# Optimization experiments

Hardware: AMD Instinct MI355X
Metric: run time of the kernel (lower is better)

## Reference

```python
import jax, jax.numpy as jnp
import numpy as np

B = 131072      # batch of states
N_ACT = 40      # output_dim (Tetris action space)


def setup_inputs() -> dict:
    key = jax.random.key(0)
    ks = jax.random.split(key, 9)
    # state vector: 11 real-valued board features, 1 hold-piece id in [0,4),
    # 3 next-piece ids in [1,8) (0 is treated as invalid by the original code)
    keep = jax.random.normal(ks[0], (B, 11), dtype=jnp.float32)
    hold = jax.random.randint(ks[1], (B, 1), 0, 4).astype(jnp.float32)
    nxt = jax.random.randint(ks[2], (B, 3), 1, 8).astype(jnp.float32)
    x = jnp.concatenate([keep, hold, nxt], axis=1)  # [B, 15]
    W1 = jax.random.normal(ks[3], (36, 128), dtype=jnp.float32) * 0.1
    b1 = jnp.zeros((128,), dtype=jnp.float32)
    W2 = jax.random.normal(ks[4], (128, 512), dtype=jnp.float32) * 0.05
    b2 = jnp.zeros((512,), dtype=jnp.float32)
    W4 = jax.random.normal(ks[5], (512, N_ACT), dtype=jnp.float32) * 0.05
    b4 = jnp.zeros((N_ACT,), dtype=jnp.float32)
    return {"x": x, "W1": W1, "b1": b1, "W2": W2, "b2": b2, "W4": W4, "b4": b4}


def reference(x, W1, b1, W2, b2, W4, b4):
    B_, _ = x.shape
    keep = x[:, :11]                                      # [B, 11]
    # vectorized replacement of the per-sample .item() one-hot loop
    hold_idx = jax.lax.stop_gradient(jnp.clip(x[:, 11].astype(jnp.int32), 0, 3))
    nxt_idx = jax.lax.stop_gradient(jnp.clip(x[:, 12:15].astype(jnp.int32) - 1, 0, 6))
    hold_oh = jax.nn.one_hot(hold_idx, 4, dtype=x.dtype)  # [B, 4]
    nxt_oh = jax.nn.one_hot(nxt_idx, 7, dtype=x.dtype).reshape(B_, 21)  # [B, 21]
    inp = jnp.concatenate([keep, hold_oh, nxt_oh], axis=1)  # [B, 36]
    h = jax.nn.relu(inp @ W1 + b1)   # [B, 128]
    h = jax.nn.relu(h @ W2 + b2)     # [B, 512]
    return h @ W4 + b4               # [B, N_ACT]
```

## Files before the change

kernel.cpp:

```cpp
#include <hip/hip_runtime.h>


typedef short bf16x8 __attribute__((ext_vector_type(8)));
typedef float f32x4 __attribute__((ext_vector_type(4)));
typedef unsigned int u32;

#define NW1F 8192
#define NW2F 65536
#define NW4F 24576
#define PACK_TOTAL (NW1F + NW2F + NW4F)
#define PACK_THREADS (PACK_TOTAL / 8)

__device__ __forceinline__ unsigned short f2bf(float f) {
  union { float f; unsigned u; } a; a.f = f;
  unsigned r = a.u + 0x7fffu + ((a.u >> 16) & 1u);
  return (unsigned short)(r >> 16);
}
__device__ __forceinline__ u32 cvtpk(float lo, float hi) {
  u32 r;
  asm("v_cvt_pk_bf16_f32 %0, %1, %2" : "=v"(r) : "v"(lo), "v"(hi));
  return r;
}

__global__ void pack_weights(const float* __restrict__ W1,
                             const float* __restrict__ W2,
                             const float* __restrict__ W4,
                             unsigned short* __restrict__ wf) {
  int t = blockIdx.x * 256 + threadIdx.x;
  if (t >= PACK_THREADS) return;
  int fid = t >> 6, lane = t & 63;
  int l16 = lane & 15, quad = lane >> 4;
  float vals[8];
  if (fid < 16) {
    int mt = fid >> 1, ks = fid & 1;
    int m = mt * 16 + l16, k0 = ks * 32 + quad * 8;
#pragma unroll
    for (int j = 0; j < 8; ++j) { int k = k0 + j; vals[j] = (k < 36) ? W1[k * 128 + m] : 0.f; }
  } else if (fid < 144) {
    int f = fid - 16, mt = f >> 2, ks = f & 3;
    int m = mt * 16 + l16, k0 = ks * 32 + quad * 8;
#pragma unroll
    for (int j = 0; j < 8; ++j) vals[j] = W2[(k0 + j) * 512 + m];
  } else {
    int f = fid - 144, mt = f >> 4, ks = f & 15;
    int m = mt * 16 + l16, k0 = ks * 32 + quad * 8;
#pragma unroll
    for (int j = 0; j < 8; ++j) vals[j] = (m < 40) ? W4[(k0 + j) * 40 + m] : 0.f;
  }
  u32 p[4];
#pragma unroll
  for (int j = 0; j < 4; ++j) p[j] = cvtpk(vals[2 * j], vals[2 * j + 1]);
  *(bf16x8*)(wf + (size_t)t * 8) = *(bf16x8*)p;
}

__global__ __launch_bounds__(128, 2) void dqn_fused(
    const float* __restrict__ x,
    const unsigned short* __restrict__ wf,
    const float* __restrict__ b1,
    const float* __restrict__ b2,
    const float* __restrict__ b4,
    float* __restrict__ out) {
  __shared__ __align__(16) unsigned short sBuf[2 * 64 * 72];

  const int tid  = threadIdx.x;
  const int lane = tid & 63;
  const int wave = tid >> 6;
  const int quad = lane >> 4;
  const int l16  = lane & 15;
  const int row0 = blockIdx.x << 7;
  const int lr0  = wave * 64;
  unsigned short* su = sBuf + wave * (64 * 72);

  const unsigned short* w2f = wf + NW1F;
  const unsigned short* w4f = wf + NW1F + NW2F;
  const unsigned short* w2p = w2f + lane * 8;

  bf16x8 curW[4];
#pragma unroll
  for (int k = 0; k < 4; ++k) curW[k] = *(const bf16x8*)(w2p + (size_t)k * 512);

  {
    const float* xr = x + (size_t)(row0 + lr0 + lane) * 15;
    unsigned short* dst = su + lane * 72;
    bf16x8 z = {0, 0, 0, 0, 0, 0, 0, 0};
#pragma unroll
    for (int c = 8; c < 64; c += 8) *(bf16x8*)(dst + c) = z;
    u32 p[4];
#pragma unroll
    for (int i = 0; i < 4; ++i) p[i] = cvtpk(xr[2 * i], xr[2 * i + 1]);
    *(bf16x8*)dst = *(bf16x8*)p;
    *(u32*)(dst + 8) = cvtpk(xr[8], xr[9]);
    dst[10] = f2bf(xr[10]);
    int hold = (int)xr[11]; hold = hold < 0 ? 0 : (hold > 3 ? 3 : hold);
    dst[11 + hold] = 0x3F80;
#pragma unroll
    for (int t = 0; t < 3; ++t) {
      int nx = (int)xr[12 + t] - 1; nx = nx < 0 ? 0 : (nx > 6 ? 6 : nx);
      dst[15 + t * 7 + nx] = 0x3F80;
    }
  }

  const f32x4 vzero = {0.f, 0.f, 0.f, 0.f};

  bf16x8 ib[4][2];
#pragma unroll
  for (int rg = 0; rg < 4; ++rg)
#pragma unroll
    for (int ks = 0; ks < 2; ++ks)
      ib[rg][ks] = *(const bf16x8*)(su + (rg * 16 + l16) * 72 + ks * 32 + quad * 8);

  bf16x8 af1[4][4];
#pragma unroll
  for (int half = 0; half < 2; ++half) {
    bf16x8 wa[4][2];
#pragma unroll
    for (int mtl = 0; mtl < 4; ++mtl)
#pragma unroll
      for (int ks = 0; ks < 2; ++ks)
        wa[mtl][ks] = *(const bf16x8*)(
            wf + (size_t)(((half * 4 + mtl) * 2 + ks) * 64 + lane) * 8);

    f32x4 acc1[4][4];
#pragma unroll
    for (int mtl = 0; mtl < 4; ++mtl)
#pragma unroll
      for (int rg = 0; rg < 4; ++rg) acc1[mtl][rg] = vzero;

#pragma unroll
    for (int mtl = 0; mtl < 4; ++mtl)
#pragma unroll
      for (int ks = 0; ks < 2; ++ks)
#pragma unroll
        for (int rg = 0; rg < 4; ++rg)
          acc1[mtl][rg] = __builtin_amdgcn_mfma_f32_16x16x32_bf16(wa[mtl][ks], ib[rg][ks], acc1[mtl][rg], 0, 0, 0);

#pragma unroll
    for (int mtl = 0; mtl < 4; ++mtl) {
      f32x4 bias = *(const f32x4*)(b1 + (half * 4 + mtl) * 16 + quad * 4);
#pragma unroll
      for (int rg = 0; rg < 4; ++rg) {
        float v0 = fmaxf(acc1[mtl][rg][0] + bias[0], 0.f);
        float v1 = fmaxf(acc1[mtl][rg][1] + bias[1], 0.f);
        float v2 = fmaxf(acc1[mtl][rg][2] + bias[2], 0.f);
        float v3 = fmaxf(acc1[mtl][rg][3] + bias[3], 0.f);
        uint2 pk = {cvtpk(v0, v1), cvtpk(v2, v3)};
        *(uint2*)(su + (rg * 16 + l16) * 72 + mtl * 16 + quad * 4) = pk;
      }
    }
#pragma unroll
    for (int rg = 0; rg < 4; ++rg)
#pragma unroll
      for (int ksl = 0; ksl < 2; ++ksl)
        af1[rg][half * 2 + ksl] =
            *(const bf16x8*)(su + (rg * 16 + l16) * 72 + ksl * 32 + quad * 8);
  }

  f32x4 accO[3][4];
#pragma unroll
  for (int mt = 0; mt < 3; ++mt)
#pragma unroll
    for (int rg = 0; rg < 4; ++rg) accO[mt][rg] = vzero;

  for (int chunk = 0; chunk < 8; ++chunk) {
    bf16x8 w4r[2][3];
#pragma unroll
    for (int ks3 = 0; ks3 < 2; ++ks3)
#pragma unroll
      for (int mt3 = 0; mt3 < 3; ++mt3)
        w4r[ks3][mt3] = *(const bf16x8*)(
            w4f + (size_t)((mt3 * 16 + chunk * 2 + ks3) * 64 + lane) * 8);

#pragma unroll
    for (int mtl = 0; mtl < 4; ++mtl) {
      int fb = chunk * 16 + mtl * 4 + 4;
      if (fb >= 128) fb = 0;
      bf16x8 nxtW[4];
#pragma unroll
      for (int k = 0; k < 4; ++k)
        nxtW[k] = *(const bf16x8*)(w2p + (size_t)(fb + k) * 512);

      f32x4 acc2[4];
#pragma unroll
      for (int rg = 0; rg < 4; ++rg) acc2[rg] = vzero;
#pragma unroll
      for (int ks = 0; ks < 4; ++ks)
#pragma unroll
        for (int rg = 0; rg < 4; ++rg)
          acc2[rg] = __builtin_amdgcn_mfma_f32_16x16x32_bf16(curW[ks], af1[rg][ks], acc2[rg], 0, 0, 0);

      f32x4 bias = *(const f32x4*)(b2 + chunk * 64 + mtl * 16 + quad * 4);
#pragma unroll
      for (int rg = 0; rg < 4; ++rg) {
        float v0 = fmaxf(acc2[rg][0] + bias[0], 0.f);
        float v1 = fmaxf(acc2[rg][1] + bias[1], 0.f);
        float v2 = fmaxf(acc2[rg][2] + bias[2], 0.f);
        float v3 = fmaxf(acc2[rg][3] + bias[3], 0.f);
        uint2 pk = {cvtpk(v0, v1), cvtpk(v2, v3)};
        *(uint2*)(su + (rg * 16 + l16) * 72 + mtl * 16 + quad * 4) = pk;
      }
#pragma unroll
      for (int k = 0; k < 4; ++k) curW[k] = nxtW[k];
    }

#pragma unroll
    for (int ks3 = 0; ks3 < 2; ++ks3) {
      bf16x8 h[4];
#pragma unroll
      for (int rg = 0; rg < 4; ++rg)
        h[rg] = *(const bf16x8*)(su + (rg * 16 + l16) * 72 + ks3 * 32 + quad * 8);
#pragma unroll
      for (int mt3 = 0; mt3 < 3; ++mt3)
#pragma unroll
        for (int rg = 0; rg < 4; ++rg)
          accO[mt3][rg] = __builtin_amdgcn_mfma_f32_16x16x32_bf16(w4r[ks3][mt3], h[rg], accO[mt3][rg], 0, 0, 0);
    }
  }

#pragma unroll
  for (int mt3 = 0; mt3 < 3; ++mt3) {
    int colbase = mt3 * 16 + quad * 4;
    if (colbase < 40) {
      f32x4 bias = *(const f32x4*)(b4 + colbase);
#pragma unroll
      for (int rg = 0; rg < 4; ++rg) {
        f32x4 v = accO[mt3][rg] + bias;
        size_t row = (size_t)(row0 + lr0 + rg * 16 + l16);
        *(f32x4*)(out + row * 40 + colbase) = v;
      }
    }
  }
}

extern "C" void kernel_launch(void* const* d_in, const int* in_sizes, int n_in,
                              void* d_out, int out_size, void* d_ws, size_t ws_size,
                              hipStream_t stream) {
  const float* x  = (const float*)d_in[0];
  const float* W1 = (const float*)d_in[1];
  const float* b1 = (const float*)d_in[2];
  const float* W2 = (const float*)d_in[3];
  const float* b2 = (const float*)d_in[4];
  const float* W4 = (const float*)d_in[5];
  const float* b4 = (const float*)d_in[6];
  float* out = (float*)d_out;
  unsigned short* wf = (unsigned short*)d_ws;

  int B = in_sizes[0] / 15;

  hipLaunchKernelGGL(pack_weights, dim3((PACK_THREADS + 255) / 256), dim3(256), 0, stream,
                     W1, W2, W4, wf);
  hipLaunchKernelGGL(dqn_fused, dim3(B / 128), dim3(128), 0, stream,
                     x, wf, b1, b2, b4, out);
}
```

Before: 99.53 us.

## Double-buffer layer-2 activations and overlap layer-3 MFMAs with next chunk

Doubles the per-wave LDS activation buffer so each chunk's layer-2 output goes to one buffer while the previous chunk's output is read from the other. The layer-3 MFMAs for the previous chunk are interleaved into the middle of the current chunk's layer-2 loop, with a final drain after the loop. Biases are also folded into the accumulator initial values instead of being added after the MFMAs. The aim is to hide LDS read latency and the serial layer-3 tail behind layer-2 work, at the cost of twice the LDS and extra registers for the held activation fragments.

```diff
diff --git a/kernel.cpp b/kernel.cpp
--- a/kernel.cpp
+++ b/kernel.cpp
@@ -60,7 +60,7 @@
     const float* __restrict__ b2,
     const float* __restrict__ b4,
     float* __restrict__ out) {
-  __shared__ __align__(16) unsigned short sBuf[2 * 64 * 72];
+  __shared__ __align__(16) unsigned short sBuf[2 * 2 * 4608];
 
   const int tid  = threadIdx.x;
   const int lane = tid & 63;
@@ -69,7 +69,7 @@
   const int l16  = lane & 15;
   const int row0 = blockIdx.x << 7;
   const int lr0  = wave * 64;
-  unsigned short* su = sBuf + wave * (64 * 72);
+  unsigned short* su = sBuf + wave * (2 * 4608);
 
   const unsigned short* w2f = wf + NW1F;
   const unsigned short* w4f = wf + NW1F + NW2F;
@@ -100,8 +100,6 @@
     }
   }
 
-  const f32x4 vzero = {0.f, 0.f, 0.f, 0.f};
-
   bf16x8 ib[4][2];
 #pragma unroll
   for (int rg = 0; rg < 4; ++rg)
@@ -122,9 +120,11 @@
 
     f32x4 acc1[4][4];
 #pragma unroll
-    for (int mtl = 0; mtl < 4; ++mtl)
-#pragma unroll
-      for (int rg = 0; rg < 4; ++rg) acc1[mtl][rg] = vzero;
+    for (int mtl = 0; mtl < 4; ++mtl) {
+      f32x4 bias = *(const f32x4*)(b1 + (half * 4 + mtl) * 16 + quad * 4);
+#pragma unroll
+      for (int rg = 0; rg < 4; ++rg) acc1[mtl][rg] = bias;
+    }
 
 #pragma unroll
     for (int mtl = 0; mtl < 4; ++mtl)
@@ -135,18 +135,16 @@
           acc1[mtl][rg] = __builtin_amdgcn_mfma_f32_16x16x32_bf16(wa[mtl][ks], ib[rg][ks], acc1[mtl][rg], 0, 0, 0);
 
 #pragma unroll
-    for (int mtl = 0; mtl < 4; ++mtl) {
-      f32x4 bias = *(const f32x4*)(b1 + (half * 4 + mtl) * 16 + quad * 4);
-#pragma unroll
-      for (int rg = 0; rg < 4; ++rg) {
-        float v0 = fmaxf(acc1[mtl][rg][0] + bias[0], 0.f);
-        float v1 = fmaxf(acc1[mtl][rg][1] + bias[1], 0.f);
-        float v2 = fmaxf(acc1[mtl][rg][2] + bias[2], 0.f);
-        float v3 = fmaxf(acc1[mtl][rg][3] + bias[3], 0.f);
+    for (int mtl = 0; mtl < 4; ++mtl)
+#pragma unroll
+      for (int rg = 0; rg < 4; ++rg) {
+        float v0 = fmaxf(acc1[mtl][rg][0], 0.f);
+        float v1 = fmaxf(acc1[mtl][rg][1], 0.f);
+        float v2 = fmaxf(acc1[mtl][rg][2], 0.f);
+        float v3 = fmaxf(acc1[mtl][rg][3], 0.f);
         uint2 pk = {cvtpk(v0, v1), cvtpk(v2, v3)};
         *(uint2*)(su + (rg * 16 + l16) * 72 + mtl * 16 + quad * 4) = pk;
       }
-    }
 #pragma unroll
     for (int rg = 0; rg < 4; ++rg)
 #pragma unroll
@@ -157,18 +155,31 @@
 
   f32x4 accO[3][4];
 #pragma unroll
-  for (int mt = 0; mt < 3; ++mt)
-#pragma unroll
-    for (int rg = 0; rg < 4; ++rg) accO[mt][rg] = vzero;
-
+  for (int mt3 = 0; mt3 < 3; ++mt3) {
+    int colbase = mt3 * 16 + quad * 4;
+    f32x4 bias = *(const f32x4*)(b4 + (colbase < 40 ? colbase : 36));
+#pragma unroll
+    for (int rg = 0; rg < 4; ++rg) accO[mt3][rg] = bias;
+  }
+
+  bf16x8 w4r[2][3];
+  bf16x8 hp[8];
   for (int chunk = 0; chunk < 8; ++chunk) {
-    bf16x8 w4r[2][3];
-#pragma unroll
-    for (int ks3 = 0; ks3 < 2; ++ks3)
-#pragma unroll
-      for (int mt3 = 0; mt3 < 3; ++mt3)
-        w4r[ks3][mt3] = *(const bf16x8*)(
-            w4f + (size_t)((mt3 * 16 + chunk * 2 + ks3) * 64 + lane) * 8);
+    unsigned short* ubuf = su + (chunk & 1) * 4608;
+    const unsigned short* rbuf = su + ((chunk & 1) ^ 1) * 4608;
+    if (chunk > 0) {
+      int pc = chunk - 1;
+#pragma unroll
+      for (int ks3 = 0; ks3 < 2; ++ks3)
+#pragma unroll
+        for (int mt3 = 0; mt3 < 3; ++mt3)
+          w4r[ks3][mt3] = *(const bf16x8*)(
+              w4f + (size_t)((mt3 * 16 + pc * 2 + ks3) * 64 + lane) * 8);
+    }
+    f32x4 b2v[4];
+#pragma unroll
+    for (int mtl = 0; mtl < 4; ++mtl)
+      b2v[mtl] = *(const f32x4*)(b2 + chunk * 64 + mtl * 16 + quad * 4);
 
 #pragma unroll
     for (int mtl = 0; mtl < 4; ++mtl) {
@@ -181,38 +192,67 @@
 
       f32x4 acc2[4];
 #pragma unroll
-      for (int rg = 0; rg < 4; ++rg) acc2[rg] = vzero;
+      for (int rg = 0; rg < 4; ++rg) acc2[rg] = b2v[mtl];
 #pragma unroll
       for (int ks = 0; ks < 4; ++ks)
 #pragma unroll
         for (int rg = 0; rg < 4; ++rg)
           acc2[rg] = __builtin_amdgcn_mfma_f32_16x16x32_bf16(curW[ks], af1[rg][ks], acc2[rg], 0, 0, 0);
 
-      f32x4 bias = *(const f32x4*)(b2 + chunk * 64 + mtl * 16 + quad * 4);
-#pragma unroll
-      for (int rg = 0; rg < 4; ++rg) {
-        float v0 = fmaxf(acc2[rg][0] + bias[0], 0.f);
-        float v1 = fmaxf(acc2[rg][1] + bias[1], 0.f);
-        float v2 = fmaxf(acc2[rg][2] + bias[2], 0.f);
-        float v3 = fmaxf(acc2[rg][3] + bias[3], 0.f);
+      if (chunk > 0 && mtl == 1) {
+#pragma unroll
+        for (int ks3 = 0; ks3 < 2; ++ks3)
+#pragma unroll
+          for (int rg = 0; rg < 4; ++rg)
+            hp[ks3 * 4 + rg] = *(const bf16x8*)(
+                rbuf + (rg * 16 + l16) * 72 + ks3 * 32 + quad * 8);
+      }
+      if (chunk > 0 && mtl == 2) {
+#pragma unroll
+        for (int mt3 = 0; mt3 < 3; ++mt3)
+#pragma unroll
+          for (int rg = 0; rg < 4; ++rg)
+            accO[mt3][rg] = __builtin_amdgcn_mfma_f32_16x16x32_bf16(w4r[0][mt3], hp[rg], accO[mt3][rg], 0, 0, 0);
+      }
+      if (chunk > 0 && mtl == 3) {
+#pragma unroll
+        for (int mt3 = 0; mt3 < 3; ++mt3)
+#pragma unroll
+          for (int rg = 0; rg < 4; ++rg)
+            accO[mt3][rg] = __builtin_amdgcn_mfma_f32_16x16x32_bf16(w4r[1][mt3], hp[4 + rg], accO[mt3][rg], 0, 0, 0);
+      }
+
+#pragma unroll
+      for (int rg = 0; rg < 4; ++rg) {
+        float v0 = fmaxf(acc2[rg][0], 0.f);
+        float v1 = fmaxf(acc2[rg][1], 0.f);
+        float v2 = fmaxf(acc2[rg][2], 0.f);
+        float v3 = fmaxf(acc2[rg][3], 0.f);
         uint2 pk = {cvtpk(v0, v1), cvtpk(v2, v3)};
-        *(uint2*)(su + (rg * 16 + l16) * 72 + mtl * 16 + quad * 4) = pk;
+        *(uint2*)(ubuf + (rg * 16 + l16) * 72 + mtl * 16 + quad * 4) = pk;
       }
 #pragma unroll
       for (int k = 0; k < 4; ++k) curW[k] = nxtW[k];
     }
-
+  }
+
+  {
+    const unsigned short* rbuf = su + 4608;
+#pragma unroll
+    for (int ks3 = 0; ks3 < 2; ++ks3)
+#pragma unroll
+      for (int mt3 = 0; mt3 < 3; ++mt3)
+        w4r[ks3][mt3] = *(const bf16x8*)(
+            w4f + (size_t)((mt3 * 16 + 7 * 2 + ks3) * 64 + lane) * 8);
 #pragma unroll
     for (int ks3 = 0; ks3 < 2; ++ks3) {
-      bf16x8 h[4];
-#pragma unroll
-      for (int rg = 0; rg < 4; ++rg)
-        h[rg] = *(const bf16x8*)(su + (rg * 16 + l16) * 72 + ks3 * 32 + quad * 8);
-#pragma unroll
-      for (int mt3 = 0; mt3 < 3; ++mt3)
-#pragma unroll
-        for (int rg = 0; rg < 4; ++rg)
-          accO[mt3][rg] = __builtin_amdgcn_mfma_f32_16x16x32_bf16(w4r[ks3][mt3], h[rg], accO[mt3][rg], 0, 0, 0);
+#pragma unroll
+      for (int rg = 0; rg < 4; ++rg) {
+        bf16x8 h = *(const bf16x8*)(rbuf + (rg * 16 + l16) * 72 + ks3 * 32 + quad * 8);
+#pragma unroll
+        for (int mt3 = 0; mt3 < 3; ++mt3)
+          accO[mt3][rg] = __builtin_amdgcn_mfma_f32_16x16x32_bf16(w4r[ks3][mt3], h, accO[mt3][rg], 0, 0, 0);
+      }
     }
   }
 
@@ -220,12 +260,10 @@
   for (int mt3 = 0; mt3 < 3; ++mt3) {
     int colbase = mt3 * 16 + quad * 4;
     if (colbase < 40) {
-      f32x4 bias = *(const f32x4*)(b4 + colbase);
-#pragma unroll
-      for (int rg = 0; rg < 4; ++rg) {
-        f32x4 v = accO[mt3][rg] + bias;
+#pragma unroll
+      for (int rg = 0; rg < 4; ++rg) {
         size_t row = (size_t)(row0 + lr0 + rg * 16 + l16);
-        *(f32x4*)(out + row * 40 + colbase) = v;
+        *(f32x4*)(out + row * 40 + colbase) = accO[mt3][rg];
       }
     }
   }
```

Result: no change. 100.1 us (+0.6%).

## Shrink per-wave tile to 32 rows and fold biases into accumulator init

Applied to the files above, without the earlier changes.

Each block becomes a single wave handling 32 rows instead of two waves handling 64 rows each, which halves the accumulator and activation register arrays and launches four times as many blocks to raise occupancy. Biases are now loaded into the MFMA accumulators as their initial values rather than added after the matmul. The trade-off is that every weight fragment loaded from global/L2 is reused over only half as many rows, so weight traffic per output row doubles.

```diff
diff --git a/kernel.cpp b/kernel.cpp
--- a/kernel.cpp
+++ b/kernel.cpp
@@ -53,23 +53,19 @@
   *(bf16x8*)(wf + (size_t)t * 8) = *(bf16x8*)p;
 }
 
-__global__ __launch_bounds__(128, 2) void dqn_fused(
+__global__ __launch_bounds__(64, 3) void dqn_fused(
     const float* __restrict__ x,
     const unsigned short* __restrict__ wf,
     const float* __restrict__ b1,
     const float* __restrict__ b2,
     const float* __restrict__ b4,
     float* __restrict__ out) {
-  __shared__ __align__(16) unsigned short sBuf[2 * 64 * 72];
-
-  const int tid  = threadIdx.x;
-  const int lane = tid & 63;
-  const int wave = tid >> 6;
+  __shared__ __align__(16) unsigned short su[32 * 72];
+
+  const int lane = threadIdx.x & 63;
   const int quad = lane >> 4;
   const int l16  = lane & 15;
-  const int row0 = blockIdx.x << 7;
-  const int lr0  = wave * 64;
-  unsigned short* su = sBuf + wave * (64 * 72);
+  const int row0 = blockIdx.x << 5;
 
   const unsigned short* w2f = wf + NW1F;
   const unsigned short* w4f = wf + NW1F + NW2F;
@@ -79,8 +75,8 @@
 #pragma unroll
   for (int k = 0; k < 4; ++k) curW[k] = *(const bf16x8*)(w2p + (size_t)k * 512);
 
-  {
-    const float* xr = x + (size_t)(row0 + lr0 + lane) * 15;
+  if (lane < 32) {
+    const float* xr = x + (size_t)(row0 + lane) * 15;
     unsigned short* dst = su + lane * 72;
     bf16x8 z = {0, 0, 0, 0, 0, 0, 0, 0};
 #pragma unroll
@@ -100,16 +96,14 @@
     }
   }
 
-  const f32x4 vzero = {0.f, 0.f, 0.f, 0.f};
-
-  bf16x8 ib[4][2];
-#pragma unroll
-  for (int rg = 0; rg < 4; ++rg)
+  bf16x8 ib[2][2];
+#pragma unroll
+  for (int rg = 0; rg < 2; ++rg)
 #pragma unroll
     for (int ks = 0; ks < 2; ++ks)
       ib[rg][ks] = *(const bf16x8*)(su + (rg * 16 + l16) * 72 + ks * 32 + quad * 8);
 
-  bf16x8 af1[4][4];
+  bf16x8 af1[2][4];
 #pragma unroll
   for (int half = 0; half < 2; ++half) {
     bf16x8 wa[4][2];
@@ -120,46 +114,48 @@
         wa[mtl][ks] = *(const bf16x8*)(
             wf + (size_t)(((half * 4 + mtl) * 2 + ks) * 64 + lane) * 8);
 
-    f32x4 acc1[4][4];
-#pragma unroll
-    for (int mtl = 0; mtl < 4; ++mtl)
-#pragma unroll
-      for (int rg = 0; rg < 4; ++rg) acc1[mtl][rg] = vzero;
-
-#pragma unroll
-    for (int mtl = 0; mtl < 4; ++mtl)
-#pragma unroll
-      for (int ks = 0; ks < 2; ++ks)
-#pragma unroll
-        for (int rg = 0; rg < 4; ++rg)
-          acc1[mtl][rg] = __builtin_amdgcn_mfma_f32_16x16x32_bf16(wa[mtl][ks], ib[rg][ks], acc1[mtl][rg], 0, 0, 0);
-
+    f32x4 acc1[4][2];
 #pragma unroll
     for (int mtl = 0; mtl < 4; ++mtl) {
       f32x4 bias = *(const f32x4*)(b1 + (half * 4 + mtl) * 16 + quad * 4);
 #pragma unroll
-      for (int rg = 0; rg < 4; ++rg) {
-        float v0 = fmaxf(acc1[mtl][rg][0] + bias[0], 0.f);
-        float v1 = fmaxf(acc1[mtl][rg][1] + bias[1], 0.f);
-        float v2 = fmaxf(acc1[mtl][rg][2] + bias[2], 0.f);
-        float v3 = fmaxf(acc1[mtl][rg][3] + bias[3], 0.f);
+      for (int rg = 0; rg < 2; ++rg) acc1[mtl][rg] = bias;
+    }
+#pragma unroll
+    for (int mtl = 0; mtl < 4; ++mtl)
+#pragma unroll
+      for (int ks = 0; ks < 2; ++ks)
+#pragma unroll
+        for (int rg = 0; rg < 2; ++rg)
+          acc1[mtl][rg] = __builtin_amdgcn_mfma_f32_16x16x32_bf16(wa[mtl][ks], ib[rg][ks], acc1[mtl][rg], 0, 0, 0);
+
+#pragma unroll
+    for (int mtl = 0; mtl < 4; ++mtl)
+#pragma unroll
+      for (int rg = 0; rg < 2; ++rg) {
+        float v0 = fmaxf(acc1[mtl][rg][0], 0.f);
+        float v1 = fmaxf(acc1[mtl][rg][1], 0.f);
+        float v2 = fmaxf(acc1[mtl][rg][2], 0.f);
+        float v3 = fmaxf(acc1[mtl][rg][3], 0.f);
         uint2 pk = {cvtpk(v0, v1), cvtpk(v2, v3)};
         *(uint2*)(su + (rg * 16 + l16) * 72 + mtl * 16 + quad * 4) = pk;
       }
-    }
-#pragma unroll
-    for (int rg = 0; rg < 4; ++rg)
+#pragma unroll
+    for (int rg = 0; rg < 2; ++rg)
 #pragma unroll
       for (int ksl = 0; ksl < 2; ++ksl)
         af1[rg][half * 2 + ksl] =
             *(const bf16x8*)(su + (rg * 16 + l16) * 72 + ksl * 32 + quad * 8);
   }
 
-  f32x4 accO[3][4];
-#pragma unroll
-  for (int mt = 0; mt < 3; ++mt)
-#pragma unroll
-    for (int rg = 0; rg < 4; ++rg) accO[mt][rg] = vzero;
+  f32x4 accO[3][2];
+#pragma unroll
+  for (int mt3 = 0; mt3 < 3; ++mt3) {
+    int colbase = mt3 * 16 + quad * 4;
+    f32x4 bias = *(const f32x4*)(b4 + (colbase < 40 ? colbase : 36));
+#pragma unroll
+    for (int rg = 0; rg < 2; ++rg) accO[mt3][rg] = bias;
+  }
 
   for (int chunk = 0; chunk < 8; ++chunk) {
     bf16x8 w4r[2][3];
@@ -179,22 +175,22 @@
       for (int k = 0; k < 4; ++k)
         nxtW[k] = *(const bf16x8*)(w2p + (size_t)(fb + k) * 512);
 
-      f32x4 acc2[4];
-#pragma unroll
-      for (int rg = 0; rg < 4; ++rg) acc2[rg] = vzero;
+      f32x4 acc2[2];
+      f32x4 b2v = *(const f32x4*)(b2 + chunk * 64 + mtl * 16 + quad * 4);
+#pragma unroll
+      for (int rg = 0; rg < 2; ++rg) acc2[rg] = b2v;
 #pragma unroll
       for (int ks = 0; ks < 4; ++ks)
 #pragma unroll
-        for (int rg = 0; rg < 4; ++rg)
+        for (int rg = 0; rg < 2; ++rg)
           acc2[rg] = __builtin_amdgcn_mfma_f32_16x16x32_bf16(curW[ks], af1[rg][ks], acc2[rg], 0, 0, 0);
 
-      f32x4 bias = *(const f32x4*)(b2 + chunk * 64 + mtl * 16 + quad * 4);
-#pragma unroll
-      for (int rg = 0; rg < 4; ++rg) {
-        float v0 = fmaxf(acc2[rg][0] + bias[0], 0.f);
-        float v1 = fmaxf(acc2[rg][1] + bias[1], 0.f);
-        float v2 = fmaxf(acc2[rg][2] + bias[2], 0.f);
-        float v3 = fmaxf(acc2[rg][3] + bias[3], 0.f);
+#pragma unroll
+      for (int rg = 0; rg < 2; ++rg) {
+        float v0 = fmaxf(acc2[rg][0], 0.f);
+        float v1 = fmaxf(acc2[rg][1], 0.f);
+        float v2 = fmaxf(acc2[rg][2], 0.f);
+        float v3 = fmaxf(acc2[rg][3], 0.f);
         uint2 pk = {cvtpk(v0, v1), cvtpk(v2, v3)};
         *(uint2*)(su + (rg * 16 + l16) * 72 + mtl * 16 + quad * 4) = pk;
       }
@@ -204,14 +200,14 @@
 
 #pragma unroll
     for (int ks3 = 0; ks3 < 2; ++ks3) {
-      bf16x8 h[4];
-#pragma unroll
-      for (int rg = 0; rg < 4; ++rg)
+      bf16x8 h[2];
+#pragma unroll
+      for (int rg = 0; rg < 2; ++rg)
         h[rg] = *(const bf16x8*)(su + (rg * 16 + l16) * 72 + ks3 * 32 + quad * 8);
 #pragma unroll
       for (int mt3 = 0; mt3 < 3; ++mt3)
 #pragma unroll
-        for (int rg = 0; rg < 4; ++rg)
+        for (int rg = 0; rg < 2; ++rg)
           accO[mt3][rg] = __builtin_amdgcn_mfma_f32_16x16x32_bf16(w4r[ks3][mt3], h[rg], accO[mt3][rg], 0, 0, 0);
     }
   }
@@ -220,12 +216,10 @@
   for (int mt3 = 0; mt3 < 3; ++mt3) {
     int colbase = mt3 * 16 + quad * 4;
     if (colbase < 40) {
-      f32x4 bias = *(const f32x4*)(b4 + colbase);
-#pragma unroll
-      for (int rg = 0; rg < 4; ++rg) {
-        f32x4 v = accO[mt3][rg] + bias;
-        size_t row = (size_t)(row0 + lr0 + rg * 16 + l16);
-        *(f32x4*)(out + row * 40 + colbase) = v;
+#pragma unroll
+      for (int rg = 0; rg < 2; ++rg) {
+        size_t row = (size_t)(row0 + rg * 16 + l16);
+        *(f32x4*)(out + row * 40 + colbase) = accO[mt3][rg];
       }
     }
   }
@@ -248,6 +242,6 @@
 
   hipLaunchKernelGGL(pack_weights, dim3((PACK_THREADS + 255) / 256), dim3(256), 0, stream,
                      W1, W2, W4, wf);
-  hipLaunchKernelGGL(dqn_fused, dim3(B / 128), dim3(128), 0, stream,
+  hipLaunchKernelGGL(dqn_fused, dim3(B / 32), dim3(64), 0, stream,
                      x, wf, b1, b2, b4, out);
 }
```

Measured after the change: 118.8 us. +19.4%, slower.
